# Kernel optimization log

Measured on AMD Instinct MI355X. Metric: run time of the kernel, lower is better.

## Reference

```python
import jax, jax.numpy as jnp
import numpy as np

B, N, H, HS = 8, 96, 8, 32
NS = H * HS  # 256, also ES
EPS = 1e-5


def _linear(x, w, b):
    return x @ w + b  # w: [in, out]


def _ln(x, g, b):
    m = jnp.mean(x, axis=-1, keepdims=True)
    v = jnp.var(x, axis=-1, keepdims=True)
    return (x - m) * jax.lax.rsqrt(v + EPS) * g + b


def _sep_n(x):  # [B,N,NS] -> [B,H,N,HS]
    b, n, _ = x.shape
    return x.reshape(b, n, H, HS).transpose(0, 2, 1, 3)


def _sep_e(x):  # [B,N,N,ES] -> [B,H,N,N,HS]
    b, n, _, _ = x.shape
    return x.reshape(b, n, n, H, HS).transpose(0, 3, 1, 2, 4)


def setup_inputs() -> dict:
    key = jax.random.key(0)
    ks = jax.random.split(key, 32)
    s = 1.0 / np.sqrt(NS)
    d = {
        "node_tensors": jax.random.normal(ks[0], (B, N, NS), jnp.float32),
        "edge_tensors": jax.random.normal(ks[1], (B, N, N, NS), jnp.float32),
    }
    names = ["Wn", "We", "Wn1", "Wn2", "Wee"]
    for i, nm in enumerate(names):
        d[nm + "_w"] = jax.random.uniform(ks[2 + 2 * i], (3, NS, NS), jnp.float32, -s, s)
        d[nm + "_b"] = jax.random.uniform(ks[3 + 2 * i], (3, NS), jnp.float32, -s, s)
    for i, nm in enumerate(["NL1", "NL2", "EL1", "EL2"]):
        d[nm + "_w"] = jax.random.uniform(ks[12 + 2 * i], (NS, NS), jnp.float32, -s, s)
        d[nm + "_b"] = jax.random.uniform(ks[13 + 2 * i], (NS,), jnp.float32, -s, s)
    d["NLN1_g"] = jnp.ones((NS,), jnp.float32)
    d["NLN1_b"] = jnp.zeros((NS,), jnp.float32)
    d["ELN1_g"] = jnp.ones((NS,), jnp.float32)
    d["ELN1_b"] = jnp.zeros((NS,), jnp.float32)
    return d


def _forward(node_tensors, edge_tensors, Wn_w, Wn_b, We_w, We_b, Wn1_w, Wn1_b,
             Wn2_w, Wn2_b, Wee_w, Wee_b, NL1_w, NL1_b, NL2_w, NL2_b,
             EL1_w, EL1_b, EL2_w, EL2_b, NLN1_g, NLN1_b, ELN1_g, ELN1_b):
    scale = 1.0 / jnp.sqrt(jnp.float32(HS))
    b = node_tensors.shape[0]

    # --- node attention ---
    eQ = _sep_e(_linear(edge_tensors, We_w[0], We_b[0]))
    eK = _sep_e(_linear(edge_tensors, We_w[1], We_b[1]))
    eV = _sep_e(_linear(edge_tensors, We_w[2], We_b[2]))
    nQ = _sep_n(_linear(node_tensors, Wn_w[0], Wn_b[0]))
    nK = _sep_n(_linear(node_tensors, Wn_w[1], Wn_b[1]))
    nV = _sep_n(_linear(node_tensors, Wn_w[2], Wn_b[2]))

    Q = eQ + nQ[:, :, :, None, :]          # [B,H,N,N,HS]
    K = eK + nK[:, :, None, :, :]
    scores = jnp.einsum('bhijc,bhijc->bhij', Q, K) * scale
    attn = jax.nn.softmax(scores, axis=-1)
    V = eV + nV[:, :, None, :, :]
    new_nodes = jnp.einsum('bhij,bhijc->bhic', attn, V)   # [B,H,N,HS]
    attw = new_nodes.transpose(0, 2, 1, 3).reshape(b, N, NS)

    res = _linear(jax.nn.relu(_linear(attw, NL1_w, NL1_b)), NL2_w, NL2_b)
    node_out = _ln(node_tensors + res, NLN1_g, NLN1_b)

    # --- edge update ---
    n1Q = _sep_n(_linear(node_out, Wn1_w[0], Wn1_b[0]))
    n1K = _sep_n(_linear(node_out, Wn1_w[1], Wn1_b[1]))
    n1V = _sep_n(_linear(node_out, Wn1_w[2], Wn1_b[2]))
    n2Q = _sep_n(_linear(node_out, Wn2_w[0], Wn2_b[0]))
    n2K = _sep_n(_linear(node_out, Wn2_w[1], Wn2_b[1]))
    n2V = _sep_n(_linear(node_out, Wn2_w[2], Wn2_b[2]))
    eQe = _sep_e(_linear(edge_tensors, Wee_w[0], Wee_b[0]))
    eKe = _sep_e(_linear(edge_tensors, Wee_w[1], Wee_b[1]))
    eVe = _sep_e(_linear(edge_tensors, Wee_w[2], Wee_b[2]))

    Qe = eQe + n1Q[:, :, :, None, :] + n2Q[:, :, None, :, :]
    Ke = eKe + n1K[:, :, :, None, :] + n2K[:, :, None, :, :]
    se = jnp.einsum('bhijc,bhijc->bhij', Qe, Ke) * scale
    attn_e = jax.nn.silu(se)                               # [B,H,N,N]
    Ve = eVe + n1V[:, :, :, None, :] + n2V[:, :, None, :, :]
    new_edges = attn_e[..., None] * Ve                     # [B,H,N,N,HS]
    attw_e = new_edges.transpose(0, 2, 3, 1, 4).reshape(b, N, N, NS)

    res_e = _linear(jax.nn.relu(_linear(attw_e, EL1_w, EL1_b)), EL2_w, EL2_b)
    edge_out = _ln(edge_tensors + res_e, ELN1_g, ELN1_b)
    return node_out, edge_out


def reference(node_tensors, edge_tensors, Wn_w, Wn_b, We_w, We_b, Wn1_w, Wn1_b,
              Wn2_w, Wn2_b, Wee_w, Wee_b, NL1_w, NL1_b, NL2_w, NL2_b,
              EL1_w, EL1_b, EL2_w, EL2_b, NLN1_g, NLN1_b, ELN1_g, ELN1_b):
    return _forward(node_tensors, edge_tensors, Wn_w, Wn_b, We_w, We_b,
                    Wn1_w, Wn1_b, Wn2_w, Wn2_b, Wee_w, Wee_b, NL1_w, NL1_b,
                    NL2_w, NL2_b, EL1_w, EL1_b, EL2_w, EL2_b,
                    NLN1_g, NLN1_b, ELN1_g, ELN1_b)
```

## Files before the change

### kernel.cpp

```cpp
#include <hip/hip_runtime.h>


#define DI __device__ __forceinline__

typedef float f32x4 __attribute__((ext_vector_type(4)));
typedef short bf16x8 __attribute__((ext_vector_type(8)));

DI unsigned short f2bf(float f) {
  union { float f; unsigned u; } v; v.f = f;
  return (unsigned short)((v.u + 0x7FFFu + ((v.u >> 16) & 1u)) >> 16);
}
DI float bf2f(unsigned short h) {
  union { unsigned u; float f; } v; v.u = ((unsigned)h) << 16;
  return v.f;
}

#define LDE 264
#define SCALE 0.17677669529663687f

#define MFMA(A, B, C) __builtin_amdgcn_mfma_f32_16x16x32_bf16((A), (B), (C), 0, 0, 0)

__global__ __launch_bounds__(256)
void prep_and_qkv(const float* __restrict__ We_w, const float* __restrict__ Wee_w,
                  const float* __restrict__ EL1_w, const float* __restrict__ EL2_w,
                  unsigned short* __restrict__ fb,
                  const float* __restrict__ node, const float* __restrict__ Ww,
                  const float* __restrict__ Wb, float* __restrict__ nQ,
                  float* __restrict__ nK, float* __restrict__ nV)
{
  __shared__ float Wl[32 * 256];
  const int t = threadIdx.x;
  if (blockIdx.x < 64) {
    const int blk = blockIdx.x, kt = blk & 7, ms = blk >> 3;
    const float* src; unsigned short* dst; int NT, ntbase;
    if (ms < 3)       { src = We_w  + ms * 65536;       dst = fb;          NT = 48; ntbase = ms * 16; }
    else if (ms < 6)  { src = Wee_w + (ms - 3) * 65536; dst = fb + 196608; NT = 48; ntbase = (ms - 3) * 16; }
    else if (ms == 6) { src = EL1_w;                    dst = fb + 393216; NT = 16; ntbase = 0; }
    else              { src = EL2_w;                    dst = fb + 458752; NT = 16; ntbase = 0; }
    for (int u = t; u < 32 * 64; u += 256) {
      const int r = u >> 6, c4 = (u & 63) << 2;
      *(float4*)(Wl + r * 256 + c4) = *(const float4*)(src + (kt * 32 + r) * 256 + c4);
    }
    __syncthreads();
    for (int u = t; u < 16 * 64; u += 256) {
      const int ntl = u >> 6, l = u & 63;
      const int kb = (l >> 4) << 3, c = ntl * 16 + (l & 15);
      unsigned short tmp[8];
      #pragma unroll
      for (int i = 0; i < 8; ++i) tmp[i] = f2bf(Wl[(kb + i) * 256 + c]);
      const int nt = ntbase + ntl;
      *(uint4*)(dst + ((size_t)(kt * NT + nt) * 64 + l) * 8) = *(const uint4*)tmp;
    }
  } else {
    float (*x)[256] = (float(*)[256])Wl;
    const int r0 = (blockIdx.x - 64) * 4;
    #pragma unroll
    for (int rr = 0; rr < 4; ++rr) x[rr][t] = node[(r0 + rr) * 256 + t];
    __syncthreads();
    float a0[4], a1[4], a2[4];
    #pragma unroll
    for (int rr = 0; rr < 4; ++rr) { a0[rr] = Wb[t]; a1[rr] = Wb[256 + t]; a2[rr] = Wb[512 + t]; }
    for (int k = 0; k < 256; ++k) {
      const float w0 = Ww[k * 256 + t], w1 = Ww[65536 + k * 256 + t], w2 = Ww[131072 + k * 256 + t];
      #pragma unroll
      for (int rr = 0; rr < 4; ++rr) {
        const float xv = x[rr][k];
        a0[rr] += xv * w0; a1[rr] += xv * w1; a2[rr] += xv * w2;
      }
    }
    const int h = t >> 5, c = t & 31;
    #pragma unroll
    for (int rr = 0; rr < 4; ++rr) {
      const int row = r0 + rr, b = row / 96, j = row - b * 96;
      const int oi = ((b * 8 + h) * 96 + j) * 32 + c;
      nQ[oi] = a0[rr]; nK[oi] = a1[rr]; nV[oi] = a2[rr];
    }
  }
}

__global__ __launch_bounds__(512, 2)
void node_attn(const float* __restrict__ edge, const float* __restrict__ We_b,
               const unsigned short* __restrict__ WeF,
               const float* __restrict__ nQ, const float* __restrict__ nK,
               const float* __restrict__ nV, float* __restrict__ attw)
{
  __shared__ unsigned short Elds[96 * LDE];
  __shared__ float sc[768];
  __shared__ float nQp[256];
  __shared__ float bias[768];

  const int tid = threadIdx.x, lane = tid & 63, wid = tid >> 6;
  const int b = blockIdx.x & 7, i = blockIdx.x >> 3;
  const size_t bi = (size_t)(b * 96 + i);

  if (tid < 256) nQp[tid] = nQ[((b * 8 + (tid >> 5)) * 96 + i) * 32 + (tid & 31)];
  for (int u = tid; u < 768; u += 512) bias[u] = We_b[u];

  const float* Erow = edge + bi * 24576;
  for (int u = tid; u < 96 * 64; u += 512) {
    const int j = u >> 6, g = u & 63;
    const float4 v = *(const float4*)(Erow + j * 256 + g * 4);
    const unsigned lo = (unsigned)f2bf(v.x) | ((unsigned)f2bf(v.y) << 16);
    const unsigned hi = (unsigned)f2bf(v.z) | ((unsigned)f2bf(v.w) << 16);
    *(uint2*)(Elds + j * LDE + g * 4) = make_uint2(lo, hi);
  }
  __syncthreads();

  {
    const int h = wid;
    const unsigned short* wq0 = WeF + ((2 * h) * 64 + lane) * 8;
    const unsigned short* wq1 = WeF + ((2 * h + 1) * 64 + lane) * 8;
    const unsigned short* wk0 = WeF + ((16 + 2 * h) * 64 + lane) * 8;
    const unsigned short* wk1 = WeF + ((17 + 2 * h) * 64 + lane) * 8;
    const int c0 = h * 32 + (lane & 15), c1 = c0 + 16;
    const float qb0 = bias[c0] + nQp[c0], qb1 = bias[c1] + nQp[c1];
    const float kb0 = bias[256 + c0], kb1 = bias[256 + c1];
    for (int pass = 0; pass < 2; ++pass) {
      const f32x4 z = {0.f, 0.f, 0.f, 0.f};
      f32x4 aq0[3] = {z, z, z}, aq1[3] = {z, z, z}, ak0[3] = {z, z, z}, ak1[3] = {z, z, z};
      __builtin_amdgcn_s_setprio(1);
      for (int kt = 0; kt < 8; ++kt) {
        const bf16x8 b0 = *(const bf16x8*)(wq0 + kt * 24576);
        const bf16x8 b1 = *(const bf16x8*)(wq1 + kt * 24576);
        const bf16x8 b2 = *(const bf16x8*)(wk0 + kt * 24576);
        const bf16x8 b3 = *(const bf16x8*)(wk1 + kt * 24576);
        #pragma unroll
        for (int m = 0; m < 3; ++m) {
          const int mt = pass * 3 + m;
          const bf16x8 afr = *(const bf16x8*)(Elds + (mt * 16 + (lane & 15)) * LDE
                                              + ((lane >> 4) << 3) + kt * 32);
          aq0[m] = MFMA(afr, b0, aq0[m]);
          aq1[m] = MFMA(afr, b1, aq1[m]);
          ak0[m] = MFMA(afr, b2, ak0[m]);
          ak1[m] = MFMA(afr, b3, ak1[m]);
        }
      }
      __builtin_amdgcn_s_setprio(0);
      #pragma unroll
      for (int m = 0; m < 3; ++m) {
        const int mt = pass * 3 + m;
        float prod[4];
        #pragma unroll
        for (int r = 0; r < 4; ++r) {
          const int j = mt * 16 + ((lane >> 4) << 2) + r;
          const int g = ((b * 8 + h) * 96 + j) * 32;
          const float k0v = ak0[m][r] + kb0 + nK[g + (lane & 15)];
          const float k1v = ak1[m][r] + kb1 + nK[g + 16 + (lane & 15)];
          prod[r] = (aq0[m][r] + qb0) * k0v + (aq1[m][r] + qb1) * k1v;
        }
        #pragma unroll
        for (int mm = 1; mm < 16; mm <<= 1) {
          #pragma unroll
          for (int r = 0; r < 4; ++r) prod[r] += __shfl_xor(prod[r], mm, 64);
        }
        if ((lane & 15) == 0) {
          #pragma unroll
          for (int r = 0; r < 4; ++r)
            sc[h * 96 + mt * 16 + ((lane >> 4) << 2) + r] = prod[r];
        }
      }
    }
  }

  const f32x4 z = {0.f, 0.f, 0.f, 0.f};
  f32x4 accB[6][2] = {{z, z}, {z, z}, {z, z}, {z, z}, {z, z}, {z, z}};
  {
    const unsigned short* wb0 = WeF + ((32 + wid) * 64 + lane) * 8;
    const unsigned short* wb1 = WeF + ((40 + wid) * 64 + lane) * 8;
    __builtin_amdgcn_s_setprio(1);
    for (int kt = 0; kt < 8; ++kt) {
      const bf16x8 b0 = *(const bf16x8*)(wb0 + kt * 24576);
      const bf16x8 b1 = *(const bf16x8*)(wb1 + kt * 24576);
      #pragma unroll
      for (int mt = 0; mt < 6; ++mt) {
        const bf16x8 afr = *(const bf16x8*)(Elds + (mt * 16 + (lane & 15)) * LDE
                                            + ((lane >> 4) << 3) + kt * 32);
        accB[mt][0] = MFMA(afr, b0, accB[mt][0]);
        accB[mt][1] = MFMA(afr, b1, accB[mt][1]);
      }
    }
    __builtin_amdgcn_s_setprio(0);
  }
  __syncthreads();

  {
    const int h = wid;
    const float s0 = sc[h * 96 + lane] * SCALE;
    const float s1 = (lane < 32) ? sc[h * 96 + 64 + lane] * SCALE : -1e30f;
    float mx = fmaxf(s0, s1);
    #pragma unroll
    for (int m = 1; m < 64; m <<= 1) mx = fmaxf(mx, __shfl_xor(mx, m, 64));
    const float e0 = __expf(s0 - mx);
    const float e1 = (lane < 32) ? __expf(s1 - mx) : 0.f;
    float sm = e0 + e1;
    #pragma unroll
    for (int m = 1; m < 64; m <<= 1) sm += __shfl_xor(sm, m, 64);
    const float inv = 1.f / sm;
    sc[h * 96 + lane] = e0 * inv;
    if (lane < 32) sc[h * 96 + 64 + lane] = e1 * inv;
  }
  __syncthreads();

  {
    const int col0 = wid * 16 + (lane & 15), col1 = col0 + 128;
    const int h0 = col0 >> 5, cc0 = col0 & 31;
    const int h1 = col1 >> 5, cc1 = col1 & 31;
    const float base0 = bias[512 + col0], base1 = bias[512 + col1];
    float nn[2] = {0.f, 0.f};
    #pragma unroll
    for (int mt = 0; mt < 6; ++mt) {
      #pragma unroll
      for (int r = 0; r < 4; ++r) {
        const int j = mt * 16 + ((lane >> 4) << 2) + r;
        const float v0 = accB[mt][0][r] + base0 + nV[((b * 8 + h0) * 96 + j) * 32 + cc0];
        const float v1 = accB[mt][1][r] + base1 + nV[((b * 8 + h1) * 96 + j) * 32 + cc1];
        nn[0] += sc[h0 * 96 + j] * v0;
        nn[1] += sc[h1 * 96 + j] * v1;
      }
    }
    #pragma unroll
    for (int s = 0; s < 2; ++s) {
      nn[s] += __shfl_xor(nn[s], 16, 64);
      nn[s] += __shfl_xor(nn[s], 32, 64);
    }
    if (lane < 16) {
      attw[bi * 256 + wid * 16 + lane] = nn[0];
      attw[bi * 256 + (wid + 8) * 16 + lane] = nn[1];
    }
  }
}

__global__ __launch_bounds__(256)
void node_tail(const float* __restrict__ attw, const float* __restrict__ node,
               const float* __restrict__ W1, const float* __restrict__ B1,
               const float* __restrict__ W2, const float* __restrict__ B2,
               const float* __restrict__ g, const float* __restrict__ be,
               const float* __restrict__ P1w, const float* __restrict__ P1b,
               const float* __restrict__ P2w, const float* __restrict__ P2b,
               float* __restrict__ node_out,
               float* __restrict__ n1Q, float* __restrict__ n1K, float* __restrict__ n1V,
               float* __restrict__ n2Q, float* __restrict__ n2K, float* __restrict__ n2V)
{
  __shared__ float xa[4][256];
  __shared__ float h1[4][256];
  __shared__ float xo[4][256];
  const int t = threadIdx.x, r0 = blockIdx.x * 4;
  #pragma unroll
  for (int rr = 0; rr < 4; ++rr) xa[rr][t] = attw[(r0 + rr) * 256 + t];
  __syncthreads();
  float acc[4];
  #pragma unroll
  for (int rr = 0; rr < 4; ++rr) acc[rr] = B1[t];
  for (int k = 0; k < 256; ++k) {
    const float w = W1[k * 256 + t];
    #pragma unroll
    for (int rr = 0; rr < 4; ++rr) acc[rr] += xa[rr][k] * w;
  }
  #pragma unroll
  for (int rr = 0; rr < 4; ++rr) h1[rr][t] = fmaxf(acc[rr], 0.f);
  __syncthreads();
  #pragma unroll
  for (int rr = 0; rr < 4; ++rr) acc[rr] = B2[t];
  for (int k = 0; k < 256; ++k) {
    const float w = W2[k * 256 + t];
    #pragma unroll
    for (int rr = 0; rr < 4; ++rr) acc[rr] += h1[rr][k] * w;
  }
  #pragma unroll
  for (int rr = 0; rr < 4; ++rr) xo[rr][t] = node[(r0 + rr) * 256 + t] + acc[rr];
  __syncthreads();
  {
    const int wid = t >> 6, lane = t & 63;
    const float4 gv = *(const float4*)(g + (lane << 2));
    const float4 bv = *(const float4*)(be + (lane << 2));
    const float4 xv = *(const float4*)(&xo[wid][lane << 2]);
    float s = xv.x + xv.y + xv.z + xv.w;
    float sq = xv.x * xv.x + xv.y * xv.y + xv.z * xv.z + xv.w * xv.w;
    #pragma unroll
    for (int m = 1; m < 64; m <<= 1) { s += __shfl_xor(s, m, 64); sq += __shfl_xor(sq, m, 64); }
    const float mean = s * (1.f / 256.f);
    const float rs = rsqrtf(sq * (1.f / 256.f) - mean * mean + 1e-5f);
    float4 o;
    o.x = (xv.x - mean) * rs * gv.x + bv.x;
    o.y = (xv.y - mean) * rs * gv.y + bv.y;
    o.z = (xv.z - mean) * rs * gv.z + bv.z;
    o.w = (xv.w - mean) * rs * gv.w + bv.w;
    *(float4*)(&xo[wid][lane << 2]) = o;
    *(float4*)(node_out + (r0 + wid) * 256 + (lane << 2)) = o;
  }
  __syncthreads();
  float a[6][4];
  #pragma unroll
  for (int rr = 0; rr < 4; ++rr) {
    a[0][rr] = P1b[t]; a[1][rr] = P1b[256 + t]; a[2][rr] = P1b[512 + t];
    a[3][rr] = P2b[t]; a[4][rr] = P2b[256 + t]; a[5][rr] = P2b[512 + t];
  }
  for (int k = 0; k < 256; ++k) {
    const float w0 = P1w[k * 256 + t], w1 = P1w[65536 + k * 256 + t], w2 = P1w[131072 + k * 256 + t];
    const float w3 = P2w[k * 256 + t], w4 = P2w[65536 + k * 256 + t], w5 = P2w[131072 + k * 256 + t];
    #pragma unroll
    for (int rr = 0; rr < 4; ++rr) {
      const float xv = xo[rr][k];
      a[0][rr] += xv * w0; a[1][rr] += xv * w1; a[2][rr] += xv * w2;
      a[3][rr] += xv * w3; a[4][rr] += xv * w4; a[5][rr] += xv * w5;
    }
  }
  const int h = t >> 5, c = t & 31;
  #pragma unroll
  for (int rr = 0; rr < 4; ++rr) {
    const int row = r0 + rr, b = row / 96, j = row - b * 96;
    const int oi = ((b * 8 + h) * 96 + j) * 32 + c;
    n1Q[oi] = a[0][rr]; n1K[oi] = a[1][rr]; n1V[oi] = a[2][rr];
    n2Q[oi] = a[3][rr]; n2K[oi] = a[4][rr]; n2V[oi] = a[5][rr];
  }
}

__global__ __launch_bounds__(512, 2)
void edge_update(const float* __restrict__ edge, const float* __restrict__ Wee_b,
                 const unsigned short* __restrict__ WeeF,
                 const unsigned short* __restrict__ EL1F,
                 const unsigned short* __restrict__ EL2F,
                 const float* __restrict__ EL1_b, const float* __restrict__ EL2_b,
                 const float* __restrict__ n1Q, const float* __restrict__ n1K, const float* __restrict__ n1V,
                 const float* __restrict__ n2Q, const float* __restrict__ n2K, const float* __restrict__ n2V,
                 const float* __restrict__ lng, const float* __restrict__ lnb,
                 float* __restrict__ edge_out)
{
  __shared__ unsigned short Elds[96 * LDE];
  __shared__ float se[768];
  __shared__ float bn1[768];
  __shared__ float b12[512];
  __shared__ float lg[256], lb[256];

  const int tid = threadIdx.x, lane = tid & 63, wid = tid >> 6;
  const int b = blockIdx.x & 7, i = blockIdx.x >> 3;
  const size_t bi = (size_t)(b * 96 + i);

  for (int u = tid; u < 768; u += 512) {
    const int q = u >> 8, cn = u & 255, h = cn >> 5, c = cn & 31;
    const float* s = (q == 0) ? n1Q : (q == 1) ? n1K : n1V;
    bn1[u] = Wee_b[u] + s[((b * 8 + h) * 96 + i) * 32 + c];
  }
  b12[tid] = (tid < 256) ? EL1_b[tid] : EL2_b[tid - 256];
  if (tid < 256) { lg[tid] = lng[tid]; lb[tid] = lnb[tid]; }

  const float* Erow = edge + bi * 24576;
  for (int u = tid; u < 96 * 64; u += 512) {
    const int j = u >> 6, g = u & 63;
    const float4 v = *(const float4*)(Erow + j * 256 + g * 4);
    const unsigned lo = (unsigned)f2bf(v.x) | ((unsigned)f2bf(v.y) << 16);
    const unsigned hi = (unsigned)f2bf(v.z) | ((unsigned)f2bf(v.w) << 16);
    *(uint2*)(Elds + j * LDE + g * 4) = make_uint2(lo, hi);
  }
  __syncthreads();

  {
    const int h = wid;
    const unsigned short* wq0 = WeeF + ((2 * h) * 64 + lane) * 8;
    const unsigned short* wq1 = WeeF + ((2 * h + 1) * 64 + lane) * 8;
    const unsigned short* wk0 = WeeF + ((16 + 2 * h) * 64 + lane) * 8;
    const unsigned short* wk1 = WeeF + ((17 + 2 * h) * 64 + lane) * 8;
    const int c0 = h * 32 + (lane & 15), c1 = c0 + 16;
    const float qb0 = bn1[c0], qb1 = bn1[c1];
    const float kb0 = bn1[256 + c0], kb1 = bn1[256 + c1];
    for (int pass = 0; pass < 2; ++pass) {
      const f32x4 z = {0.f, 0.f, 0.f, 0.f};
      f32x4 aq0[3] = {z, z, z}, aq1[3] = {z, z, z}, ak0[3] = {z, z, z}, ak1[3] = {z, z, z};
      __builtin_amdgcn_s_setprio(1);
      for (int kt = 0; kt < 8; ++kt) {
        const bf16x8 b0 = *(const bf16x8*)(wq0 + kt * 24576);
        const bf16x8 b1 = *(const bf16x8*)(wq1 + kt * 24576);
        const bf16x8 b2 = *(const bf16x8*)(wk0 + kt * 24576);
        const bf16x8 b3 = *(const bf16x8*)(wk1 + kt * 24576);
        #pragma unroll
        for (int m = 0; m < 3; ++m) {
          const int mt = pass * 3 + m;
          const bf16x8 afr = *(const bf16x8*)(Elds + (mt * 16 + (lane & 15)) * LDE
                                              + ((lane >> 4) << 3) + kt * 32);
          aq0[m] = MFMA(afr, b0, aq0[m]);
          aq1[m] = MFMA(afr, b1, aq1[m]);
          ak0[m] = MFMA(afr, b2, ak0[m]);
          ak1[m] = MFMA(afr, b3, ak1[m]);
        }
      }
      __builtin_amdgcn_s_setprio(0);
      #pragma unroll
      for (int m = 0; m < 3; ++m) {
        const int mt = pass * 3 + m;
        float prod[4];
        #pragma unroll
        for (int r = 0; r < 4; ++r) {
          const int j = mt * 16 + ((lane >> 4) << 2) + r;
          const int g = ((b * 8 + h) * 96 + j) * 32;
          const float q0v = aq0[m][r] + qb0 + n2Q[g + (lane & 15)];
          const float q1v = aq1[m][r] + qb1 + n2Q[g + 16 + (lane & 15)];
          const float k0v = ak0[m][r] + kb0 + n2K[g + (lane & 15)];
          const float k1v = ak1[m][r] + kb1 + n2K[g + 16 + (lane & 15)];
          prod[r] = q0v * k0v + q1v * k1v;
        }
        #pragma unroll
        for (int mm = 1; mm < 16; mm <<= 1) {
          #pragma unroll
          for (int r = 0; r < 4; ++r) prod[r] += __shfl_xor(prod[r], mm, 64);
        }
        if ((lane & 15) == 0) {
          #pragma unroll
          for (int r = 0; r < 4; ++r) {
            const float d = prod[r] * SCALE;
            se[h * 96 + mt * 16 + ((lane >> 4) << 2) + r] = d / (1.f + __expf(-d));
          }
        }
      }
    }
  }

  const f32x4 z = {0.f, 0.f, 0.f, 0.f};
  f32x4 acc[6][2] = {{z, z}, {z, z}, {z, z}, {z, z}, {z, z}, {z, z}};
  {
    const unsigned short* wb0 = WeeF + ((32 + wid) * 64 + lane) * 8;
    const unsigned short* wb1 = WeeF + ((40 + wid) * 64 + lane) * 8;
    __builtin_amdgcn_s_setprio(1);
    for (int kt = 0; kt < 8; ++kt) {
      const bf16x8 b0 = *(const bf16x8*)(wb0 + kt * 24576);
      const bf16x8 b1 = *(const bf16x8*)(wb1 + kt * 24576);
      #pragma unroll
      for (int mt = 0; mt < 6; ++mt) {
        const bf16x8 afr = *(const bf16x8*)(Elds + (mt * 16 + (lane & 15)) * LDE
                                            + ((lane >> 4) << 3) + kt * 32);
        acc[mt][0] = MFMA(afr, b0, acc[mt][0]);
        acc[mt][1] = MFMA(afr, b1, acc[mt][1]);
      }
    }
    __builtin_amdgcn_s_setprio(0);
  }
  __syncthreads();

  {
    const int col0 = wid * 16 + (lane & 15), col1 = col0 + 128;
    const int h0 = col0 >> 5, cc0 = col0 & 31;
    const int h1 = col1 >> 5, cc1 = col1 & 31;
    const float base0 = bn1[512 + col0], base1 = bn1[512 + col1];
    #pragma unroll
    for (int mt = 0; mt < 6; ++mt) {
      #pragma unroll
      for (int r = 0; r < 4; ++r) {
        const int j = mt * 16 + ((lane >> 4) << 2) + r;
        const float v0 = acc[mt][0][r] + base0 + n2V[((b * 8 + h0) * 96 + j) * 32 + cc0];
        const float v1 = acc[mt][1][r] + base1 + n2V[((b * 8 + h1) * 96 + j) * 32 + cc1];
        Elds[j * LDE + col0] = f2bf(se[h0 * 96 + j] * v0);
        Elds[j * LDE + col1] = f2bf(se[h1 * 96 + j] * v1);
      }
    }
  }
  __syncthreads();

  {
    #pragma unroll
    for (int mt = 0; mt < 6; ++mt) { acc[mt][0] = z; acc[mt][1] = z; }
    const unsigned short* wb0 = EL1F + (wid * 64 + lane) * 8;
    const unsigned short* wb1 = EL1F + ((wid + 8) * 64 + lane) * 8;
    __builtin_amdgcn_s_setprio(1);
    for (int kt = 0; kt < 8; ++kt) {
      const bf16x8 b0 = *(const bf16x8*)(wb0 + kt * 8192);
      const bf16x8 b1 = *(const bf16x8*)(wb1 + kt * 8192);
      #pragma unroll
      for (int mt = 0; mt < 6; ++mt) {
        const bf16x8 afr = *(const bf16x8*)(Elds + (mt * 16 + (lane & 15)) * LDE
                                            + ((lane >> 4) << 3) + kt * 32);
        acc[mt][0] = MFMA(afr, b0, acc[mt][0]);
        acc[mt][1] = MFMA(afr, b1, acc[mt][1]);
      }
    }
    __builtin_amdgcn_s_setprio(0);
    __syncthreads();
    const int col0 = wid * 16 + (lane & 15), col1 = col0 + 128;
    const float bv0 = b12[col0], bv1 = b12[col1];
    #pragma unroll
    for (int mt = 0; mt < 6; ++mt) {
      #pragma unroll
      for (int r = 0; r < 4; ++r) {
        const int j = mt * 16 + ((lane >> 4) << 2) + r;
        Elds[j * LDE + col0] = f2bf(fmaxf(acc[mt][0][r] + bv0, 0.f));
        Elds[j * LDE + col1] = f2bf(fmaxf(acc[mt][1][r] + bv1, 0.f));
      }
    }
  }
  __syncthreads();

  {
    #pragma unroll
    for (int mt = 0; mt < 6; ++mt) { acc[mt][0] = z; acc[mt][1] = z; }
    const unsigned short* wb0 = EL2F + (wid * 64 + lane) * 8;
    const unsigned short* wb1 = EL2F + ((wid + 8) * 64 + lane) * 8;
    __builtin_amdgcn_s_setprio(1);
    for (int kt = 0; kt < 8; ++kt) {
      const bf16x8 b0 = *(const bf16x8*)(wb0 + kt * 8192);
      const bf16x8 b1 = *(const bf16x8*)(wb1 + kt * 8192);
      #pragma unroll
      for (int mt = 0; mt < 6; ++mt) {
        const bf16x8 afr = *(const bf16x8*)(Elds + (mt * 16 + (lane & 15)) * LDE
                                            + ((lane >> 4) << 3) + kt * 32);
        acc[mt][0] = MFMA(afr, b0, acc[mt][0]);
        acc[mt][1] = MFMA(afr, b1, acc[mt][1]);
      }
    }
    __builtin_amdgcn_s_setprio(0);
    const int col0 = wid * 16 + (lane & 15), col1 = col0 + 128;
    const float bv0 = b12[256 + col0], bv1 = b12[256 + col1];
    const float g0 = lg[col0], g1 = lg[col1], be0 = lb[col0], be1 = lb[col1];
    __syncthreads();
    #pragma unroll
    for (int mt = 0; mt < 6; ++mt) {
      #pragma unroll
      for (int r = 0; r < 4; ++r) {
        const int j = mt * 16 + ((lane >> 4) << 2) + r;
        acc[mt][0][r] += bv0 + Erow[j * 256 + col0];
        acc[mt][1][r] += bv1 + Erow[j * 256 + col1];
      }
    }
    #pragma unroll
    for (int mt = 0; mt < 6; ++mt) {
      #pragma unroll
      for (int r = 0; r < 4; ++r) {
        float s = acc[mt][0][r] + acc[mt][1][r];
        float q = acc[mt][0][r] * acc[mt][0][r] + acc[mt][1][r] * acc[mt][1][r];
        #pragma unroll
        for (int m = 1; m < 16; m <<= 1) { s += __shfl_xor(s, m, 64); q += __shfl_xor(q, m, 64); }
        if ((lane & 15) == 0) {
          const int j = mt * 16 + ((lane >> 4) << 2) + r;
          se[wid * 96 + j] = s; bn1[wid * 96 + j] = q;
        }
      }
    }
    __syncthreads();
    if (tid < 96) {
      float s = 0.f, q = 0.f;
      #pragma unroll
      for (int w = 0; w < 8; ++w) { s += se[w * 96 + tid]; q += bn1[w * 96 + tid]; }
      const float mean = s * (1.f / 256.f);
      b12[tid] = mean;
      b12[96 + tid] = rsqrtf(q * (1.f / 256.f) - mean * mean + 1e-5f);
    }
    __syncthreads();
    #pragma unroll
    for (int mt = 0; mt < 6; ++mt) {
      #pragma unroll
      for (int r = 0; r < 4; ++r) {
        const int j = mt * 16 + ((lane >> 4) << 2) + r;
        const float mean = b12[j], rs = b12[96 + j];
        Elds[j * LDE + col0] = f2bf((acc[mt][0][r] - mean) * rs * g0 + be0);
        Elds[j * LDE + col1] = f2bf((acc[mt][1][r] - mean) * rs * g1 + be1);
      }
    }
  }
  __syncthreads();

  float* orow = edge_out + bi * 24576;
  for (int j = wid; j < 96; j += 8) {
    const uint2 pk = *(const uint2*)(Elds + j * LDE + (lane << 2));
    float4 o;
    o.x = bf2f((unsigned short)(pk.x & 0xffff));
    o.y = bf2f((unsigned short)(pk.x >> 16));
    o.z = bf2f((unsigned short)(pk.y & 0xffff));
    o.w = bf2f((unsigned short)(pk.y >> 16));
    *(float4*)(orow + j * 256 + (lane << 2)) = o;
  }
}

extern "C" void kernel_launch(void* const* d_in, const int* in_sizes, int n_in,
                              void* d_out, int out_size, void* d_ws, size_t ws_size,
                              hipStream_t stream)
{
  (void)in_sizes; (void)n_in; (void)out_size; (void)ws_size;

  const float* node   = (const float*)d_in[0];
  const float* edge   = (const float*)d_in[1];
  const float* Wn_w   = (const float*)d_in[2];
  const float* Wn_b   = (const float*)d_in[3];
  const float* We_w   = (const float*)d_in[4];
  const float* We_b   = (const float*)d_in[5];
  const float* Wn1_w  = (const float*)d_in[6];
  const float* Wn1_b  = (const float*)d_in[7];
  const float* Wn2_w  = (const float*)d_in[8];
  const float* Wn2_b  = (const float*)d_in[9];
  const float* Wee_w  = (const float*)d_in[10];
  const float* Wee_b  = (const float*)d_in[11];
  const float* NL1_w  = (const float*)d_in[12];
  const float* NL1_b  = (const float*)d_in[13];
  const float* NL2_w  = (const float*)d_in[14];
  const float* NL2_b  = (const float*)d_in[15];
  const float* EL1_w  = (const float*)d_in[16];
  const float* EL1_b  = (const float*)d_in[17];
  const float* EL2_w  = (const float*)d_in[18];
  const float* EL2_b  = (const float*)d_in[19];
  const float* NLN1_g = (const float*)d_in[20];
  const float* NLN1_b = (const float*)d_in[21];
  const float* ELN1_g = (const float*)d_in[22];
  const float* ELN1_b = (const float*)d_in[23];

  float* out = (float*)d_out;
  float* node_out = out;
  float* edge_out = out + 196608;

  float* wsf = (float*)d_ws;
  float* nQ  = wsf;                float* nK  = wsf + 196608;   float* nV  = wsf + 393216;
  float* n1Q = wsf + 589824;       float* n1K = wsf + 786432;   float* n1V = wsf + 983040;
  float* n2Q = wsf + 1179648;      float* n2K = wsf + 1376256;  float* n2V = wsf + 1572864;
  float* attw = wsf + 1769472;
  unsigned short* fb   = (unsigned short*)(wsf + 1966080);
  unsigned short* WeF  = fb;
  unsigned short* WeeF = fb + 196608;
  unsigned short* EL1F = fb + 393216;
  unsigned short* EL2F = fb + 458752;

  prep_and_qkv<<<256, 256, 0, stream>>>(We_w, Wee_w, EL1_w, EL2_w, fb,
                                        node, Wn_w, Wn_b, nQ, nK, nV);
  node_attn<<<768, 512, 0, stream>>>(edge, We_b, WeF, nQ, nK, nV, attw);
  node_tail<<<192, 256, 0, stream>>>(attw, node, NL1_w, NL1_b, NL2_w, NL2_b,
                                     NLN1_g, NLN1_b, Wn1_w, Wn1_b, Wn2_w, Wn2_b,
                                     node_out, n1Q, n1K, n1V, n2Q, n2K, n2V);
  edge_update<<<768, 512, 0, stream>>>(edge, Wee_b, WeeF, EL1F, EL2F,
                                       EL1_b, EL2_b, n1Q, n1K, n1V,
                                       n2Q, n2K, n2V, ELN1_g, ELN1_b, edge_out);
}
```

Baseline: 271.6 us.

## Move node tail MLP and projections to bf16 MFMA with pre-packed weights

Extends the weight prep kernel to convert the NL1, NL2, Wn1 and Wn2 weights into bf16 MFMA fragment layout. The node_tail kernel is rewritten to process 16 rows per block with MFMA 16x16x32 bf16 instead of scalar fp32 FMAs. LayerNorm is computed with a cross-wave partial sum reduction. This cuts fp32 scalar GEMM time in the node path at the cost of bf16 precision on the node MLP, and the grid drops to only 48 blocks.

```diff
diff --git a/kernel.cpp b/kernel.cpp
--- a/kernel.cpp
+++ b/kernel.cpp
@@ -23,6 +23,8 @@
 __global__ __launch_bounds__(256)
 void prep_and_qkv(const float* __restrict__ We_w, const float* __restrict__ Wee_w,
                   const float* __restrict__ EL1_w, const float* __restrict__ EL2_w,
+                  const float* __restrict__ NL1_w, const float* __restrict__ NL2_w,
+                  const float* __restrict__ Wn1_w, const float* __restrict__ Wn2_w,
                   unsigned short* __restrict__ fb,
                   const float* __restrict__ node, const float* __restrict__ Ww,
                   const float* __restrict__ Wb, float* __restrict__ nQ,
@@ -30,13 +32,17 @@
 {
   __shared__ float Wl[32 * 256];
   const int t = threadIdx.x;
-  if (blockIdx.x < 64) {
+  if (blockIdx.x < 128) {
     const int blk = blockIdx.x, kt = blk & 7, ms = blk >> 3;
     const float* src; unsigned short* dst; int NT, ntbase;
-    if (ms < 3)       { src = We_w  + ms * 65536;       dst = fb;          NT = 48; ntbase = ms * 16; }
-    else if (ms < 6)  { src = Wee_w + (ms - 3) * 65536; dst = fb + 196608; NT = 48; ntbase = (ms - 3) * 16; }
-    else if (ms == 6) { src = EL1_w;                    dst = fb + 393216; NT = 16; ntbase = 0; }
-    else              { src = EL2_w;                    dst = fb + 458752; NT = 16; ntbase = 0; }
+    if (ms < 3)       { src = We_w  + ms * 65536;        dst = fb;          NT = 48; ntbase = ms * 16; }
+    else if (ms < 6)  { src = Wee_w + (ms - 3) * 65536;  dst = fb + 196608; NT = 48; ntbase = (ms - 3) * 16; }
+    else if (ms == 6) { src = EL1_w;                     dst = fb + 393216; NT = 16; ntbase = 0; }
+    else if (ms == 7) { src = EL2_w;                     dst = fb + 458752; NT = 16; ntbase = 0; }
+    else if (ms == 8) { src = NL1_w;                     dst = fb + 524288; NT = 16; ntbase = 0; }
+    else if (ms == 9) { src = NL2_w;                     dst = fb + 589824; NT = 16; ntbase = 0; }
+    else if (ms < 13) { src = Wn1_w + (ms - 10) * 65536; dst = fb + 655360; NT = 48; ntbase = (ms - 10) * 16; }
+    else              { src = Wn2_w + (ms - 13) * 65536; dst = fb + 851968; NT = 48; ntbase = (ms - 13) * 16; }
     for (int u = t; u < 32 * 64; u += 256) {
       const int r = u >> 6, c4 = (u & 63) << 2;
       *(float4*)(Wl + r * 256 + c4) = *(const float4*)(src + (kt * 32 + r) * 256 + c4);
@@ -53,7 +59,7 @@
     }
   } else {
     float (*x)[256] = (float(*)[256])Wl;
-    const int r0 = (blockIdx.x - 64) * 4;
+    const int r0 = (blockIdx.x - 128) * 4;
     #pragma unroll
     for (int rr = 0; rr < 4; ++rr) x[rr][t] = node[(r0 + rr) * 256 + t];
     __syncthreads();
@@ -232,86 +238,154 @@
 
 __global__ __launch_bounds__(256)
 void node_tail(const float* __restrict__ attw, const float* __restrict__ node,
-               const float* __restrict__ W1, const float* __restrict__ B1,
-               const float* __restrict__ W2, const float* __restrict__ B2,
+               const unsigned short* __restrict__ NL1F, const float* __restrict__ B1,
+               const unsigned short* __restrict__ NL2F, const float* __restrict__ B2,
                const float* __restrict__ g, const float* __restrict__ be,
-               const float* __restrict__ P1w, const float* __restrict__ P1b,
-               const float* __restrict__ P2w, const float* __restrict__ P2b,
+               const unsigned short* __restrict__ Wn1F, const float* __restrict__ P1b,
+               const unsigned short* __restrict__ Wn2F, const float* __restrict__ P2b,
                float* __restrict__ node_out,
                float* __restrict__ n1Q, float* __restrict__ n1K, float* __restrict__ n1V,
                float* __restrict__ n2Q, float* __restrict__ n2K, float* __restrict__ n2V)
 {
-  __shared__ float xa[4][256];
-  __shared__ float h1[4][256];
-  __shared__ float xo[4][256];
-  const int t = threadIdx.x, r0 = blockIdx.x * 4;
+  __shared__ unsigned short Xl[16 * LDE];
+  __shared__ unsigned short Hl[16 * LDE];
+  __shared__ float bb[1024];
+  __shared__ float p1b[768], p2b[768];
+  __shared__ float psum[4][16], psq[4][16];
+  __shared__ float statm[16], statr[16];
+
+  const int t = threadIdx.x, lane = t & 63, w = t >> 6;
+  const int bt = blockIdx.x, r0 = bt * 16;
+  const int b = bt / 6, nbase = (bt % 6) * 16;
+
+  bb[t] = B1[t]; bb[256 + t] = B2[t]; bb[512 + t] = g[t]; bb[768 + t] = be[t];
+  for (int u = t; u < 768; u += 256) { p1b[u] = P1b[u]; p2b[u] = P2b[u]; }
+
+  for (int u = t; u < 16 * 64; u += 256) {
+    const int j = u >> 6, gg = u & 63;
+    const float4 v = *(const float4*)(attw + (size_t)(r0 + j) * 256 + gg * 4);
+    const unsigned lo = (unsigned)f2bf(v.x) | ((unsigned)f2bf(v.y) << 16);
+    const unsigned hi = (unsigned)f2bf(v.z) | ((unsigned)f2bf(v.w) << 16);
+    *(uint2*)(Xl + j * LDE + gg * 4) = make_uint2(lo, hi);
+  }
+  __syncthreads();
+
+  const f32x4 z = {0.f, 0.f, 0.f, 0.f};
+
+  {
+    f32x4 a1[4] = {z, z, z, z};
+    for (int kt = 0; kt < 8; ++kt) {
+      const bf16x8 afr = *(const bf16x8*)(Xl + (lane & 15) * LDE + ((lane >> 4) << 3) + kt * 32);
+      #pragma unroll
+      for (int p = 0; p < 4; ++p) {
+        const bf16x8 bf = *(const bf16x8*)(NL1F + (((kt << 4) + (w * 4 + p)) * 64 + lane) * 8);
+        a1[p] = MFMA(afr, bf, a1[p]);
+      }
+    }
+    #pragma unroll
+    for (int p = 0; p < 4; ++p) {
+      const int col = (w * 4 + p) * 16 + (lane & 15);
+      const float bv = bb[col];
+      #pragma unroll
+      for (int r = 0; r < 4; ++r) {
+        const int j = ((lane >> 4) << 2) + r;
+        Hl[j * LDE + col] = f2bf(fmaxf(a1[p][r] + bv, 0.f));
+      }
+    }
+  }
+  __syncthreads();
+
+  float xv[4][4];
+  {
+    f32x4 a2[4] = {z, z, z, z};
+    for (int kt = 0; kt < 8; ++kt) {
+      const bf16x8 afr = *(const bf16x8*)(Hl + (lane & 15) * LDE + ((lane >> 4) << 3) + kt * 32);
+      #pragma unroll
+      for (int p = 0; p < 4; ++p) {
+        const bf16x8 bf = *(const bf16x8*)(NL2F + (((kt << 4) + (w * 4 + p)) * 64 + lane) * 8);
+        a2[p] = MFMA(afr, bf, a2[p]);
+      }
+    }
+    #pragma unroll
+    for (int p = 0; p < 4; ++p) {
+      const int col = (w * 4 + p) * 16 + (lane & 15);
+      const float bv = bb[256 + col];
+      #pragma unroll
+      for (int r = 0; r < 4; ++r) {
+        const int j = ((lane >> 4) << 2) + r;
+        xv[p][r] = a2[p][r] + bv + node[(size_t)(r0 + j) * 256 + col];
+      }
+    }
+    #pragma unroll
+    for (int r = 0; r < 4; ++r) {
+      float s = 0.f, q = 0.f;
+      #pragma unroll
+      for (int p = 0; p < 4; ++p) { s += xv[p][r]; q += xv[p][r] * xv[p][r]; }
+      #pragma unroll
+      for (int m = 1; m < 16; m <<= 1) { s += __shfl_xor(s, m, 64); q += __shfl_xor(q, m, 64); }
+      if ((lane & 15) == 0) {
+        const int rl = ((lane >> 4) << 2) + r;
+        psum[w][rl] = s; psq[w][rl] = q;
+      }
+    }
+  }
+  __syncthreads();
+  if (t < 16) {
+    const float s = psum[0][t] + psum[1][t] + psum[2][t] + psum[3][t];
+    const float q = psq[0][t] + psq[1][t] + psq[2][t] + psq[3][t];
+    const float mean = s * (1.f / 256.f);
+    statm[t] = mean;
+    statr[t] = rsqrtf(q * (1.f / 256.f) - mean * mean + 1e-5f);
+  }
+  __syncthreads();
   #pragma unroll
-  for (int rr = 0; rr < 4; ++rr) xa[rr][t] = attw[(r0 + rr) * 256 + t];
-  __syncthreads();
-  float acc[4];
+  for (int p = 0; p < 4; ++p) {
+    const int col = (w * 4 + p) * 16 + (lane & 15);
+    const float gv = bb[512 + col], bv = bb[768 + col];
+    #pragma unroll
+    for (int r = 0; r < 4; ++r) {
+      const int j = ((lane >> 4) << 2) + r;
+      const float o = (xv[p][r] - statm[j]) * statr[j] * gv + bv;
+      node_out[(size_t)(r0 + j) * 256 + col] = o;
+      Xl[j * LDE + col] = f2bf(o);
+    }
+  }
+  __syncthreads();
+
+  bf16x8 xfr[8];
   #pragma unroll
-  for (int rr = 0; rr < 4; ++rr) acc[rr] = B1[t];
-  for (int k = 0; k < 256; ++k) {
-    const float w = W1[k * 256 + t];
-    #pragma unroll
-    for (int rr = 0; rr < 4; ++rr) acc[rr] += xa[rr][k] * w;
-  }
+  for (int kt = 0; kt < 8; ++kt)
+    xfr[kt] = *(const bf16x8*)(Xl + (lane & 15) * LDE + ((lane >> 4) << 3) + kt * 32);
   #pragma unroll
-  for (int rr = 0; rr < 4; ++rr) h1[rr][t] = fmaxf(acc[rr], 0.f);
-  __syncthreads();
-  #pragma unroll
-  for (int rr = 0; rr < 4; ++rr) acc[rr] = B2[t];
-  for (int k = 0; k < 256; ++k) {
-    const float w = W2[k * 256 + t];
-    #pragma unroll
-    for (int rr = 0; rr < 4; ++rr) acc[rr] += h1[rr][k] * w;
-  }
-  #pragma unroll
-  for (int rr = 0; rr < 4; ++rr) xo[rr][t] = node[(r0 + rr) * 256 + t] + acc[rr];
-  __syncthreads();
-  {
-    const int wid = t >> 6, lane = t & 63;
-    const float4 gv = *(const float4*)(g + (lane << 2));
-    const float4 bv = *(const float4*)(be + (lane << 2));
-    const float4 xv = *(const float4*)(&xo[wid][lane << 2]);
-    float s = xv.x + xv.y + xv.z + xv.w;
-    float sq = xv.x * xv.x + xv.y * xv.y + xv.z * xv.z + xv.w * xv.w;
-    #pragma unroll
-    for (int m = 1; m < 64; m <<= 1) { s += __shfl_xor(s, m, 64); sq += __shfl_xor(sq, m, 64); }
-    const float mean = s * (1.f / 256.f);
-    const float rs = rsqrtf(sq * (1.f / 256.f) - mean * mean + 1e-5f);
-    float4 o;
-    o.x = (xv.x - mean) * rs * gv.x + bv.x;
-    o.y = (xv.y - mean) * rs * gv.y + bv.y;
-    o.z = (xv.z - mean) * rs * gv.z + bv.z;
-    o.w = (xv.w - mean) * rs * gv.w + bv.w;
-    *(float4*)(&xo[wid][lane << 2]) = o;
-    *(float4*)(node_out + (r0 + wid) * 256 + (lane << 2)) = o;
-  }
-  __syncthreads();
-  float a[6][4];
-  #pragma unroll
-  for (int rr = 0; rr < 4; ++rr) {
-    a[0][rr] = P1b[t]; a[1][rr] = P1b[256 + t]; a[2][rr] = P1b[512 + t];
-    a[3][rr] = P2b[t]; a[4][rr] = P2b[256 + t]; a[5][rr] = P2b[512 + t];
-  }
-  for (int k = 0; k < 256; ++k) {
-    const float w0 = P1w[k * 256 + t], w1 = P1w[65536 + k * 256 + t], w2 = P1w[131072 + k * 256 + t];
-    const float w3 = P2w[k * 256 + t], w4 = P2w[65536 + k * 256 + t], w5 = P2w[131072 + k * 256 + t];
-    #pragma unroll
-    for (int rr = 0; rr < 4; ++rr) {
-      const float xv = xo[rr][k];
-      a[0][rr] += xv * w0; a[1][rr] += xv * w1; a[2][rr] += xv * w2;
-      a[3][rr] += xv * w3; a[4][rr] += xv * w4; a[5][rr] += xv * w5;
-    }
-  }
-  const int h = t >> 5, c = t & 31;
-  #pragma unroll
-  for (int rr = 0; rr < 4; ++rr) {
-    const int row = r0 + rr, b = row / 96, j = row - b * 96;
-    const int oi = ((b * 8 + h) * 96 + j) * 32 + c;
-    n1Q[oi] = a[0][rr]; n1K[oi] = a[1][rr]; n1V[oi] = a[2][rr];
-    n2Q[oi] = a[3][rr]; n2K[oi] = a[4][rr]; n2V[oi] = a[5][rr];
+  for (int ps = 0; ps < 2; ++ps) {
+    const unsigned short* WF = ps ? Wn2F : Wn1F;
+    const float* pb = ps ? p2b : p1b;
+    f32x4 ac[12] = {z, z, z, z, z, z, z, z, z, z, z, z};
+    __builtin_amdgcn_s_setprio(1);
+    for (int kt = 0; kt < 8; ++kt) {
+      #pragma unroll
+      for (int m = 0; m < 12; ++m) {
+        const int nt = w * 12 + m;
+        const bf16x8 bf = *(const bf16x8*)(WF + ((kt * 48 + nt) * 64 + lane) * 8);
+        ac[m] = MFMA(xfr[kt], bf, ac[m]);
+      }
+    }
+    __builtin_amdgcn_s_setprio(0);
+    #pragma unroll
+    for (int m = 0; m < 12; ++m) {
+      const int nt = w * 12 + m;
+      const int colg = nt * 16 + (lane & 15);
+      const int q = colg >> 8, cn = colg & 255, h = cn >> 5, c = cn & 31;
+      float* o = (q == 0) ? (ps ? n2Q : n1Q)
+               : (q == 1) ? (ps ? n2K : n1K)
+                          : (ps ? n2V : n1V);
+      const float bv = pb[colg];
+      #pragma unroll
+      for (int r = 0; r < 4; ++r) {
+        const int j = ((lane >> 4) << 2) + r;
+        o[((b * 8 + h) * 96 + nbase + j) * 32 + c] = ac[m][r] + bv;
+      }
+    }
   }
 }
 
@@ -612,13 +686,18 @@
   unsigned short* WeeF = fb + 196608;
   unsigned short* EL1F = fb + 393216;
   unsigned short* EL2F = fb + 458752;
-
-  prep_and_qkv<<<256, 256, 0, stream>>>(We_w, Wee_w, EL1_w, EL2_w, fb,
+  unsigned short* NL1F = fb + 524288;
+  unsigned short* NL2F = fb + 589824;
+  unsigned short* Wn1F = fb + 655360;
+  unsigned short* Wn2F = fb + 851968;
+
+  prep_and_qkv<<<320, 256, 0, stream>>>(We_w, Wee_w, EL1_w, EL2_w,
+                                        NL1_w, NL2_w, Wn1_w, Wn2_w, fb,
                                         node, Wn_w, Wn_b, nQ, nK, nV);
   node_attn<<<768, 512, 0, stream>>>(edge, We_b, WeF, nQ, nK, nV, attw);
-  node_tail<<<192, 256, 0, stream>>>(attw, node, NL1_w, NL1_b, NL2_w, NL2_b,
-                                     NLN1_g, NLN1_b, Wn1_w, Wn1_b, Wn2_w, Wn2_b,
-                                     node_out, n1Q, n1K, n1V, n2Q, n2K, n2V);
+  node_tail<<<48, 256, 0, stream>>>(attw, node, NL1F, NL1_b, NL2F, NL2_b,
+                                    NLN1_g, NLN1_b, Wn1F, Wn1_b, Wn2F, Wn2_b,
+                                    node_out, n1Q, n1K, n1V, n2Q, n2K, n2V);
   edge_update<<<768, 512, 0, stream>>>(edge, Wee_b, WeeF, EL1F, EL2F,
                                        EL1_b, EL2_b, n1Q, n1K, n1V,
                                        n2Q, n2K, n2V, ELN1_g, ELN1_b, edge_out);
```

Result: faster. 261.4 us (-3.8%).
